# Performance work log

Measured on AMD Instinct MI355X. Metric: run time of the kernel, lower is better.

Reference implementation:

```python
import jax, jax.numpy as jnp
import numpy as np
import math

B, S, H = 2, 2048, 1024
NH, HD = 16, 64  # num heads, head dim; NH*HD == H


def setup_inputs() -> dict:
    key = jax.random.key(0)
    k1, k2, k3 = jax.random.split(key, 3)
    hidden_states = jax.random.normal(k1, (B, S, H), dtype=jnp.float32)
    # causal multiplicative mask [1,1,S,S], 1.0 where attending is allowed
    mask = jnp.tril(jnp.ones((S, S), dtype=jnp.float32))[None, None]
    W_qkv = jax.random.normal(k2, (H, 3 * H), dtype=jnp.float32) * (1.0 / math.sqrt(H))
    b_qkv = jnp.zeros((3 * H,), dtype=jnp.float32)
    W_out = jax.random.normal(k3, (H, H), dtype=jnp.float32) * (1.0 / math.sqrt(H))
    b_out = jnp.zeros((H,), dtype=jnp.float32)
    return {"hidden_states": hidden_states, "mask": mask, "W_qkv": W_qkv,
            "b_qkv": b_qkv, "W_out": W_out, "b_out": b_out}


def reference(hidden_states, mask, W_qkv, b_qkv, W_out, b_out):
    b, s, h = hidden_states.shape
    # fused QKV projection then split into contiguous thirds (split_tensor_along_last_dim)
    qkv = jnp.einsum('bsh,hd->bsd', hidden_states, W_qkv) + b_qkv
    q, k, v = jnp.split(qkv, 3, axis=-1)
    # [b, s, nh*hd] -> [b, nh, s, hd]
    def to_heads(t):
        return t.reshape(b, s, NH, HD).transpose(0, 2, 1, 3)
    q, k, v = to_heads(q), to_heads(k), to_heads(v)
    q = q / jnp.sqrt(jnp.float32(HD))  # scaling_attention_score=True
    scores = jnp.einsum('bhqd,bhkd->bhqk', q, k)  # [b,nh,s,s]
    # multiplicative mask + large-negative bias trick from standard_attention
    scores = scores * mask - 10000.0 * (1.0 - mask)
    probs = jax.nn.softmax(scores, axis=-1)
    ctx = jnp.einsum('bhqk,bhkd->bhqd', probs, v)
    ctx = ctx.transpose(0, 2, 1, 3).reshape(b, s, h)  # [b, s, nh*hd]
    return jnp.einsum('bsh,hd->bsd', ctx, W_out) + b_out
```

## Files before the change

kernel.cpp:

```cpp
#include <hip/hip_runtime.h>
#include <cstdint>
#include <cstddef>

#define NHEAD 16
#define HDIM 64
#define SEQ 2048
#define BATCH 2
#define HID 1024

typedef __bf16 bf16x8 __attribute__((ext_vector_type(8)));
typedef float f32x4 __attribute__((ext_vector_type(4)));

__device__ __forceinline__ unsigned short f2bf(float f) {
    union { float f; unsigned u; } v; v.f = f;
    unsigned r = v.u + 0x7fffu + ((v.u >> 16) & 1u);
    return (unsigned short)(r >> 16);
}

__global__ __launch_bounds__(256) void convert_f32_bf16(
    const float* __restrict__ in, unsigned short* __restrict__ out, int n) {
    int i = (blockIdx.x * 256 + threadIdx.x) * 8;
    if (i >= n) return;
    float4 a = *(const float4*)(in + i);
    float4 b = *(const float4*)(in + i + 4);
    uint4 o;
    o.x = (unsigned)f2bf(a.x) | ((unsigned)f2bf(a.y) << 16);
    o.y = (unsigned)f2bf(a.z) | ((unsigned)f2bf(a.w) << 16);
    o.z = (unsigned)f2bf(b.x) | ((unsigned)f2bf(b.y) << 16);
    o.w = (unsigned)f2bf(b.z) | ((unsigned)f2bf(b.w) << 16);
    *(uint4*)(out + i) = o;
}

__global__ __launch_bounds__(256) void transpose_f32_bf16(
    const float* __restrict__ in, unsigned short* __restrict__ out, int R, int C) {
    __shared__ unsigned short T[64][72];
    int t = threadIdx.x;
    int c0 = blockIdx.x * 64, r0 = blockIdx.y * 64;
    for (int p = 0; p < 4; ++p) {
        int idx = (p * 256 + t) * 4;
        int row = idx >> 6, col = idx & 63;
        float4 v = *(const float4*)(in + (size_t)(r0 + row) * C + c0 + col);
        T[row][col + 0] = f2bf(v.x);
        T[row][col + 1] = f2bf(v.y);
        T[row][col + 2] = f2bf(v.z);
        T[row][col + 3] = f2bf(v.w);
    }
    __syncthreads();
    for (int p = 0; p < 4; ++p) {
        int idx = (p * 256 + t) * 4;
        int orow = idx >> 6, ocol = idx & 63;
        ushort4 u;
        u.x = T[ocol + 0][orow];
        u.y = T[ocol + 1][orow];
        u.z = T[ocol + 2][orow];
        u.w = T[ocol + 3][orow];
        *(ushort4*)(out + (size_t)(c0 + orow) * R + r0 + ocol) = u;
    }
}

__global__ __launch_bounds__(256) void transpose_v(
    const unsigned short* __restrict__ in, unsigned short* __restrict__ out) {
    __shared__ unsigned short T[64][72];
    int t = threadIdx.x;
    int s0 = blockIdx.x * 64, bh = blockIdx.y;
    const unsigned short* ip = in + (size_t)bh * SEQ * HDIM;
    unsigned short* op = out + (size_t)bh * HDIM * SEQ;
    for (int p = 0; p < 2; ++p) {
        int idx = (p * 256 + t) * 8;
        int row = idx >> 6, col = idx & 63;
        *(uint4*)&T[row][col] = *(const uint4*)(ip + (size_t)(s0 + row) * HDIM + col);
    }
    __syncthreads();
    for (int p = 0; p < 4; ++p) {
        int idx = (p * 256 + t) * 4;
        int d = idx >> 6, c = idx & 63;
        ushort4 u;
        u.x = T[c + 0][d];
        u.y = T[c + 1][d];
        u.z = T[c + 2][d];
        u.w = T[c + 3][d];
        *(ushort4*)(op + (size_t)d * SEQ + s0 + c) = u;
    }
}

#define GEMM_BODY(Aptr, Btptr, KDIM)                                                     \
    __shared__ unsigned short As[128][32];                                               \
    __shared__ unsigned short Bs[128][32];                                               \
    int t = threadIdx.x;                                                                 \
    int wave = t >> 6, lane = t & 63, ln = lane & 15, quad = lane >> 4;                  \
    int wm = wave >> 1, wn = wave & 1;                                                   \
    int m0 = blockIdx.y * 128, n0 = blockIdx.x * 128;                                    \
    int srow = lane >> 2, scol = (lane & 3) * 8;                                         \
    f32x4 zero4 = {0.f, 0.f, 0.f, 0.f};                                                  \
    f32x4 acc[4][4];                                                                     \
    for (int mi = 0; mi < 4; ++mi)                                                       \
        for (int ni = 0; ni < 4; ++ni) acc[mi][ni] = zero4;                              \
    for (int kt = 0; kt < (KDIM); kt += 32) {                                            \
        for (int p = 0; p < 2; ++p) {                                                    \
            int r0 = (wave * 2 + p) * 16 + srow;                                         \
            __builtin_amdgcn_global_load_lds(                                            \
                (const __attribute__((address_space(1))) void*)                          \
                    ((Aptr) + (size_t)(m0 + r0) * (KDIM) + kt + scol),                   \
                (__attribute__((address_space(3))) void*)&As[(wave * 2 + p) * 16][0],    \
                16, 0, 0);                                                               \
            __builtin_amdgcn_global_load_lds(                                            \
                (const __attribute__((address_space(1))) void*)                          \
                    ((Btptr) + (size_t)(n0 + r0) * (KDIM) + kt + scol),                  \
                (__attribute__((address_space(3))) void*)&Bs[(wave * 2 + p) * 16][0],    \
                16, 0, 0);                                                               \
        }                                                                                \
        __syncthreads();                                                                 \
        bf16x8 af[4], bfr[4];                                                            \
        for (int mi = 0; mi < 4; ++mi)                                                   \
            af[mi] = *(const bf16x8*)&As[wm * 64 + mi * 16 + ln][quad * 8];              \
        for (int ni = 0; ni < 4; ++ni)                                                   \
            bfr[ni] = *(const bf16x8*)&Bs[wn * 64 + ni * 16 + ln][quad * 8];             \
        for (int mi = 0; mi < 4; ++mi)                                                   \
            for (int ni = 0; ni < 4; ++ni)                                               \
                acc[mi][ni] = __builtin_amdgcn_mfma_f32_16x16x32_bf16(                   \
                    af[mi], bfr[ni], acc[mi][ni], 0, 0, 0);                              \
        __syncthreads();                                                                 \
    }

__global__ __launch_bounds__(256) void gemm_qkv(
    const unsigned short* __restrict__ A, const unsigned short* __restrict__ Bt,
    const float* __restrict__ bias,
    unsigned short* __restrict__ Qb, unsigned short* __restrict__ Kb,
    unsigned short* __restrict__ Vtmp) {
    GEMM_BODY(A, Bt, 1024)
    int nbase = n0 + wn * 64;
    for (int ni = 0; ni < 4; ++ni) {
        int gn = nbase + ni * 16 + ln;
        float bv = bias[gn];
        int third = gn >> 10;
        int rem = gn & 1023;
        int h = rem >> 6, d = rem & 63;
        unsigned short* dst = third == 0 ? Qb : (third == 1 ? Kb : Vtmp);
        float scale = third == 0 ? 0.1803368801111f : 1.0f;
        for (int mi = 0; mi < 4; ++mi) {
            for (int r = 0; r < 4; ++r) {
                int gm = m0 + wm * 64 + mi * 16 + quad * 4 + r;
                int b = gm >> 11, s = gm & 2047;
                size_t bh = (size_t)(b * NHEAD + h);
                dst[(bh * SEQ + s) * HDIM + d] = f2bf((acc[mi][ni][r] + bv) * scale);
            }
        }
    }
}

__global__ __launch_bounds__(256) void gemm_out(
    const unsigned short* __restrict__ A, const unsigned short* __restrict__ Bt,
    const float* __restrict__ bias, float* __restrict__ C) {
    GEMM_BODY(A, Bt, 1024)
    int nbase = n0 + wn * 64;
    for (int ni = 0; ni < 4; ++ni) {
        int gn = nbase + ni * 16 + ln;
        float bv = bias[gn];
        for (int mi = 0; mi < 4; ++mi) {
            for (int r = 0; r < 4; ++r) {
                int gm = m0 + wm * 64 + mi * 16 + quad * 4 + r;
                C[(size_t)gm * HID + gn] = acc[mi][ni][r] + bv;
            }
        }
    }
}

__global__ __launch_bounds__(256) void flash_attn(
    const unsigned short* __restrict__ Qb, const unsigned short* __restrict__ Kb,
    const unsigned short* __restrict__ Vt, unsigned short* __restrict__ Ctx) {
    __shared__ unsigned short KsB[2][64][64];
    __shared__ unsigned short VsB[2][64][64];
    __shared__ unsigned short Ps[4][16][72];
    int tid = threadIdx.x;
    int wave = tid >> 6, lane = tid & 63, ln = lane & 15, quad = lane >> 4;
    int bx = blockIdx.x, bh = blockIdx.y;
    int qiA = bx;
    int q0A = qiA * 64, q0B = (31 - bx) * 64;
    const size_t baseQK = (size_t)bh * SEQ * HDIM;
    const size_t baseV = (size_t)bh * HDIM * SEQ;
    int b = bh >> 4, h = bh & 15;

    int rIn = lane >> 3;
    int gsw = ((lane & 7) ^ rIn) * 8;

    bf16x8 aqA0, aqA1, aqB0, aqB1;
    {
        const unsigned short* qp =
            Qb + baseQK + (size_t)(q0A + wave * 16 + ln) * HDIM + quad * 8;
        aqA0 = *(const bf16x8*)qp;
        aqA1 = *(const bf16x8*)(qp + 32);
        qp = Qb + baseQK + (size_t)(q0B + wave * 16 + ln) * HDIM + quad * 8;
        aqB0 = *(const bf16x8*)qp;
        aqB1 = *(const bf16x8*)(qp + 32);
    }
    bf16x8 aqc0 = aqA0, aqc1 = aqA1;

    auto prefetch = [&](int kj, int bi) {
        const unsigned short* kb = Kb + baseQK + (size_t)kj * 64 * HDIM;
        const unsigned short* vb = Vt + baseV + kj * 64;
        for (int c = wave; c < 8; c += 4) {
            __builtin_amdgcn_global_load_lds(
                (const __attribute__((address_space(1))) void*)(kb + (c * 8 + rIn) * HDIM + gsw),
                (__attribute__((address_space(3))) void*)&KsB[bi][c * 8][0], 16, 0, 0);
            __builtin_amdgcn_global_load_lds(
                (const __attribute__((address_space(1))) void*)(vb + (size_t)(c * 8 + rIn) * SEQ + gsw),
                (__attribute__((address_space(3))) void*)&VsB[bi][c * 8][0], 16, 0, 0);
        }
    };

    f32x4 zero4 = {0.f, 0.f, 0.f, 0.f};
    f32x4 o[4];
    float lacc = 0.f;
    for (int i = 0; i < 4; ++i) o[i] = zero4;

    prefetch(0, 0);
    for (int t = 0; t <= 32; ++t) {
        __syncthreads();
        if (t < 32) {
            int kn = (t + 1 <= qiA) ? (t + 1) : (t - qiA);
            prefetch(kn, (t + 1) & 1);
        }
        int buf = t & 1;
        bool diag = (t == qiA) || (t == 32);

        f32x4 s4[4];
        for (int ni = 0; ni < 4; ++ni) s4[ni] = zero4;
        for (int kk = 0; kk < 2; ++kk) {
            bf16x8 bq = kk ? aqc1 : aqc0;
            for (int ni = 0; ni < 4; ++ni) {
                bf16x8 ak = *(const bf16x8*)
                    &KsB[buf][ni * 16 + ln][(((kk * 4 + quad)) ^ (ln & 7)) * 8];
                s4[ni] = __builtin_amdgcn_mfma_f32_16x16x32_bf16(ak, bq, s4[ni], 0, 0, 0);
            }
        }
        if (diag) {
            for (int ni = 0; ni < 4; ++ni)
                for (int r = 0; r < 4; ++r)
                    if (ni * 16 + quad * 4 + r > wave * 16 + ln) s4[ni][r] = -1.0e38f;
        }

        for (int ni = 0; ni < 4; ++ni) {
            float e0 = __builtin_amdgcn_exp2f(s4[ni][0]);
            float e1 = __builtin_amdgcn_exp2f(s4[ni][1]);
            float e2 = __builtin_amdgcn_exp2f(s4[ni][2]);
            float e3 = __builtin_amdgcn_exp2f(s4[ni][3]);
            lacc += (e0 + e1) + (e2 + e3);
            ushort4 pk;
            pk.x = f2bf(e0); pk.y = f2bf(e1); pk.z = f2bf(e2); pk.w = f2bf(e3);
            *(ushort4*)&Ps[wave][ln][ni * 16 + quad * 4] = pk;
        }

        for (int kk = 0; kk < 2; ++kk) {
            bf16x8 bp = *(const bf16x8*)&Ps[wave][ln][kk * 32 + quad * 8];
            for (int ni = 0; ni < 4; ++ni) {
                bf16x8 av = *(const bf16x8*)
                    &VsB[buf][ni * 16 + ln][(((kk * 4 + quad)) ^ (ln & 7)) * 8];
                o[ni] = __builtin_amdgcn_mfma_f32_16x16x32_bf16(av, bp, o[ni], 0, 0, 0);
            }
        }

        if (diag) {
            float sum = lacc;
            sum += __shfl_xor(sum, 16);
            sum += __shfl_xor(sum, 32);
            float linv = __builtin_amdgcn_rcpf(sum);
            int q0 = (t == 32) ? q0B : q0A;
            size_t rowb = ((size_t)(b * SEQ + q0 + wave * 16 + ln)) * HID + h * 64;
            for (int ni = 0; ni < 4; ++ni) {
                ushort4 u;
                u.x = f2bf(o[ni][0] * linv);
                u.y = f2bf(o[ni][1] * linv);
                u.z = f2bf(o[ni][2] * linv);
                u.w = f2bf(o[ni][3] * linv);
                *(ushort4*)&Ctx[rowb + ni * 16 + quad * 4] = u;
            }
            for (int i = 0; i < 4; ++i) o[i] = zero4;
            lacc = 0.f;
            aqc0 = aqB0;
            aqc1 = aqB1;
        }
    }
}

extern "C" void kernel_launch(void* const* d_in, const int* in_sizes, int n_in,
                              void* d_out, int out_size, void* d_ws, size_t ws_size,
                              hipStream_t stream) {
    const float* X = (const float*)d_in[0];
    const float* Wqkv = (const float*)d_in[2];
    const float* bqkv = (const float*)d_in[3];
    const float* Wout = (const float*)d_in[4];
    const float* bout = (const float*)d_in[5];
    float* out = (float*)d_out;

    char* ws = (char*)d_ws;
    unsigned short* Xb   = (unsigned short*)(ws + 0);
    unsigned short* Vt   = (unsigned short*)(ws + 0);
    unsigned short* W1t  = (unsigned short*)(ws + 8388608);
    unsigned short* W2t  = (unsigned short*)(ws + 14680064);
    unsigned short* Qb   = (unsigned short*)(ws + 16777216);
    unsigned short* Kb   = (unsigned short*)(ws + 25165824);
    unsigned short* Vtmp = (unsigned short*)(ws + 33554432);
    unsigned short* Ctx  = (unsigned short*)(ws + 41943040);

    convert_f32_bf16<<<2048, 256, 0, stream>>>(X, Xb, 4194304);
    transpose_f32_bf16<<<dim3(48, 16), 256, 0, stream>>>(Wqkv, W1t, 1024, 3072);
    transpose_f32_bf16<<<dim3(16, 16), 256, 0, stream>>>(Wout, W2t, 1024, 1024);
    gemm_qkv<<<dim3(24, 32), 256, 0, stream>>>(Xb, W1t, bqkv, Qb, Kb, Vtmp);
    transpose_v<<<dim3(32, 32), 256, 0, stream>>>(Vtmp, Vt);
    flash_attn<<<dim3(16, 32), 256, 0, stream>>>(Qb, Kb, Vt, Ctx);
    gemm_out<<<dim3(8, 32), 256, 0, stream>>>(Ctx, W2t, bout, out);
}
```

Before: 209.4 us.

## Fuse V transpose into QKV GEMM, process paired query tiles jointly, remap blocks per XCD

The QKV GEMM epilogue now writes V directly in transposed layout, which removes the separate transpose_v kernel and its extra global round trip. The flash attention kernel now handles its two query tiles at the same time, so each K/V tile is loaded once and reused by both, where before the K range was walked twice in sequence. It also hoists the fragment loads, adds setprio around the MFMA blocks, uses the packed bf16 convert instruction, and sets launch bounds for two blocks per CU. All three main kernels remap block IDs so that neighbouring tiles land on the same XCD, aiming for better L2 reuse. Keeping both accumulators live raises register pressure, and the transposed V stores are narrow and strided.

```diff
diff --git a/kernel.cpp b/kernel.cpp
--- a/kernel.cpp
+++ b/kernel.cpp
@@ -15,6 +15,12 @@
     union { float f; unsigned u; } v; v.f = f;
     unsigned r = v.u + 0x7fffu + ((v.u >> 16) & 1u);
     return (unsigned short)(r >> 16);
+}
+
+__device__ __forceinline__ unsigned cvtpk_bf16(float a, float b) {
+    unsigned d;
+    asm("v_cvt_pk_bf16_f32 %0, %1, %2" : "=v"(d) : "v"(a), "v"(b));
+    return d;
 }
 
 __global__ __launch_bounds__(256) void convert_f32_bf16(
@@ -58,38 +64,13 @@
     }
 }
 
-__global__ __launch_bounds__(256) void transpose_v(
-    const unsigned short* __restrict__ in, unsigned short* __restrict__ out) {
-    __shared__ unsigned short T[64][72];
-    int t = threadIdx.x;
-    int s0 = blockIdx.x * 64, bh = blockIdx.y;
-    const unsigned short* ip = in + (size_t)bh * SEQ * HDIM;
-    unsigned short* op = out + (size_t)bh * HDIM * SEQ;
-    for (int p = 0; p < 2; ++p) {
-        int idx = (p * 256 + t) * 8;
-        int row = idx >> 6, col = idx & 63;
-        *(uint4*)&T[row][col] = *(const uint4*)(ip + (size_t)(s0 + row) * HDIM + col);
-    }
-    __syncthreads();
-    for (int p = 0; p < 4; ++p) {
-        int idx = (p * 256 + t) * 4;
-        int d = idx >> 6, c = idx & 63;
-        ushort4 u;
-        u.x = T[c + 0][d];
-        u.y = T[c + 1][d];
-        u.z = T[c + 2][d];
-        u.w = T[c + 3][d];
-        *(ushort4*)(op + (size_t)d * SEQ + s0 + c) = u;
-    }
-}
-
-#define GEMM_BODY(Aptr, Btptr, KDIM)                                                     \
+#define GEMM_BODY(Aptr, Btptr, KDIM, BX, BY)                                             \
     __shared__ unsigned short As[128][32];                                               \
     __shared__ unsigned short Bs[128][32];                                               \
     int t = threadIdx.x;                                                                 \
     int wave = t >> 6, lane = t & 63, ln = lane & 15, quad = lane >> 4;                  \
     int wm = wave >> 1, wn = wave & 1;                                                   \
-    int m0 = blockIdx.y * 128, n0 = blockIdx.x * 128;                                    \
+    int m0 = (BY) * 128, n0 = (BX) * 128;                                                \
     int srow = lane >> 2, scol = (lane & 3) * 8;                                         \
     f32x4 zero4 = {0.f, 0.f, 0.f, 0.f};                                                  \
     f32x4 acc[4][4];                                                                     \
@@ -126,8 +107,12 @@
     const unsigned short* __restrict__ A, const unsigned short* __restrict__ Bt,
     const float* __restrict__ bias,
     unsigned short* __restrict__ Qb, unsigned short* __restrict__ Kb,
-    unsigned short* __restrict__ Vtmp) {
-    GEMM_BODY(A, Bt, 1024)
+    unsigned short* __restrict__ Vt) {
+    int fid = blockIdx.y * 24 + blockIdx.x;
+    int xcd = fid & 7, jj = fid >> 3;
+    int by = (xcd & 3) * 8 + jj / 12;
+    int bx = (xcd >> 2) * 12 + jj % 12;
+    GEMM_BODY(A, Bt, 1024, bx, by)
     int nbase = n0 + wn * 64;
     for (int ni = 0; ni < 4; ++ni) {
         int gn = nbase + ni * 16 + ln;
@@ -135,14 +120,28 @@
         int third = gn >> 10;
         int rem = gn & 1023;
         int h = rem >> 6, d = rem & 63;
-        unsigned short* dst = third == 0 ? Qb : (third == 1 ? Kb : Vtmp);
-        float scale = third == 0 ? 0.1803368801111f : 1.0f;
-        for (int mi = 0; mi < 4; ++mi) {
-            for (int r = 0; r < 4; ++r) {
-                int gm = m0 + wm * 64 + mi * 16 + quad * 4 + r;
+        if (third == 2) {
+            for (int mi = 0; mi < 4; ++mi) {
+                int gm = m0 + wm * 64 + mi * 16 + quad * 4;
                 int b = gm >> 11, s = gm & 2047;
                 size_t bh = (size_t)(b * NHEAD + h);
-                dst[(bh * SEQ + s) * HDIM + d] = f2bf((acc[mi][ni][r] + bv) * scale);
+                ushort4 u;
+                u.x = f2bf(acc[mi][ni][0] + bv);
+                u.y = f2bf(acc[mi][ni][1] + bv);
+                u.z = f2bf(acc[mi][ni][2] + bv);
+                u.w = f2bf(acc[mi][ni][3] + bv);
+                *(ushort4*)&Vt[(bh * HDIM + d) * SEQ + s] = u;
+            }
+        } else {
+            unsigned short* dst = third == 0 ? Qb : Kb;
+            float scale = third == 0 ? 0.1803368801111f : 1.0f;
+            for (int mi = 0; mi < 4; ++mi) {
+                for (int r = 0; r < 4; ++r) {
+                    int gm = m0 + wm * 64 + mi * 16 + quad * 4 + r;
+                    int b = gm >> 11, s = gm & 2047;
+                    size_t bh = (size_t)(b * NHEAD + h);
+                    dst[(bh * SEQ + s) * HDIM + d] = f2bf((acc[mi][ni][r] + bv) * scale);
+                }
             }
         }
     }
@@ -151,7 +150,11 @@
 __global__ __launch_bounds__(256) void gemm_out(
     const unsigned short* __restrict__ A, const unsigned short* __restrict__ Bt,
     const float* __restrict__ bias, float* __restrict__ C) {
-    GEMM_BODY(A, Bt, 1024)
+    int fid = blockIdx.y * 8 + blockIdx.x;
+    int xcd = fid & 7, jj = fid >> 3;
+    int by = xcd * 4 + (jj >> 3);
+    int bx = jj & 7;
+    GEMM_BODY(A, Bt, 1024, bx, by)
     int nbase = n0 + wn * 64;
     for (int ni = 0; ni < 4; ++ni) {
         int gn = nbase + ni * 16 + ln;
@@ -165,17 +168,23 @@
     }
 }
 
-__global__ __launch_bounds__(256) void flash_attn(
+__global__ __launch_bounds__(256, 2) void flash_attn(
     const unsigned short* __restrict__ Qb, const unsigned short* __restrict__ Kb,
     const unsigned short* __restrict__ Vt, unsigned short* __restrict__ Ctx) {
     __shared__ unsigned short KsB[2][64][64];
     __shared__ unsigned short VsB[2][64][64];
-    __shared__ unsigned short Ps[4][16][72];
+    __shared__ unsigned short Ps[2][4][16][72];
     int tid = threadIdx.x;
     int wave = tid >> 6, lane = tid & 63, ln = lane & 15, quad = lane >> 4;
-    int bx = blockIdx.x, bh = blockIdx.y;
-    int qiA = bx;
-    int q0A = qiA * 64, q0B = (31 - bx) * 64;
+
+    int id = blockIdx.y * 16 + blockIdx.x;
+    int xcd = id & 7, j = id >> 3;
+    int bh = xcd * 4 + (j & 3);
+    int r0 = (j >> 2) & 7;
+    int bxrole = (j < 32) ? r0 : 15 - r0;
+    int qiA = bxrole;
+    int qiB = 31 - bxrole;
+    int q0A = qiA * 64, q0B = qiB * 64;
     const size_t baseQK = (size_t)bh * SEQ * HDIM;
     const size_t baseV = (size_t)bh * HDIM * SEQ;
     int b = bh >> 4, h = bh & 15;
@@ -193,7 +202,6 @@
         aqB0 = *(const bf16x8*)qp;
         aqB1 = *(const bf16x8*)(qp + 32);
     }
-    bf16x8 aqc0 = aqA0, aqc1 = aqA1;
 
     auto prefetch = [&](int kj, int bi) {
         const unsigned short* kb = Kb + baseQK + (size_t)kj * 64 * HDIM;
@@ -209,76 +217,138 @@
     };
 
     f32x4 zero4 = {0.f, 0.f, 0.f, 0.f};
-    f32x4 o[4];
-    float lacc = 0.f;
-    for (int i = 0; i < 4; ++i) o[i] = zero4;
+    f32x4 oA[4], oB[4];
+    float laccA = 0.f, laccB = 0.f;
+    for (int i = 0; i < 4; ++i) { oA[i] = zero4; oB[i] = zero4; }
+
+    auto epilogue = [&](const f32x4* o, float lacc, int q0) {
+        float sum = lacc;
+        sum += __shfl_xor(sum, 16);
+        sum += __shfl_xor(sum, 32);
+        float linv = __builtin_amdgcn_rcpf(sum);
+        size_t rowb = ((size_t)(b * SEQ + q0 + wave * 16 + ln)) * HID + h * 64;
+        for (int ni = 0; ni < 4; ++ni) {
+            ushort4 u;
+            u.x = f2bf(o[ni][0] * linv);
+            u.y = f2bf(o[ni][1] * linv);
+            u.z = f2bf(o[ni][2] * linv);
+            u.w = f2bf(o[ni][3] * linv);
+            *(ushort4*)&Ctx[rowb + ni * 16 + quad * 4] = u;
+        }
+    };
 
     prefetch(0, 0);
-    for (int t = 0; t <= 32; ++t) {
+    for (int t = 0; t <= qiB; ++t) {
         __syncthreads();
-        if (t < 32) {
-            int kn = (t + 1 <= qiA) ? (t + 1) : (t - qiA);
-            prefetch(kn, (t + 1) & 1);
-        }
+        if (t < qiB) prefetch(t + 1, (t + 1) & 1);
         int buf = t & 1;
-        bool diag = (t == qiA) || (t == 32);
-
-        f32x4 s4[4];
-        for (int ni = 0; ni < 4; ++ni) s4[ni] = zero4;
+        bool joint = (t <= qiA);
+
+        bf16x8 akf[2][4];
+#pragma unroll
+        for (int kk = 0; kk < 2; ++kk)
+#pragma unroll
+            for (int ni = 0; ni < 4; ++ni)
+                akf[kk][ni] = *(const bf16x8*)
+                    &KsB[buf][ni * 16 + ln][((kk * 4 + quad) ^ (ln & 7)) * 8];
+        f32x4 sA[4], sB[4];
+#pragma unroll
+        for (int ni = 0; ni < 4; ++ni) { sA[ni] = zero4; sB[ni] = zero4; }
+        __builtin_amdgcn_s_setprio(1);
+#pragma unroll
         for (int kk = 0; kk < 2; ++kk) {
-            bf16x8 bq = kk ? aqc1 : aqc0;
+            bf16x8 bq = kk ? aqB1 : aqB0;
+#pragma unroll
+            for (int ni = 0; ni < 4; ++ni)
+                sB[ni] = __builtin_amdgcn_mfma_f32_16x16x32_bf16(akf[kk][ni], bq, sB[ni], 0, 0, 0);
+        }
+        if (joint) {
+#pragma unroll
+            for (int kk = 0; kk < 2; ++kk) {
+                bf16x8 bq = kk ? aqA1 : aqA0;
+#pragma unroll
+                for (int ni = 0; ni < 4; ++ni)
+                    sA[ni] = __builtin_amdgcn_mfma_f32_16x16x32_bf16(akf[kk][ni], bq, sA[ni], 0, 0, 0);
+            }
+        }
+        __builtin_amdgcn_s_setprio(0);
+
+        if (t == qiB) {
+#pragma unroll
+            for (int ni = 0; ni < 4; ++ni)
+#pragma unroll
+                for (int r = 0; r < 4; ++r)
+                    if (ni * 16 + quad * 4 + r > wave * 16 + ln) sB[ni][r] = -1.0e38f;
+        }
+        if (t == qiA) {
+#pragma unroll
+            for (int ni = 0; ni < 4; ++ni)
+#pragma unroll
+                for (int r = 0; r < 4; ++r)
+                    if (ni * 16 + quad * 4 + r > wave * 16 + ln) sA[ni][r] = -1.0e38f;
+        }
+
+#pragma unroll
+        for (int ni = 0; ni < 4; ++ni) {
+            float e0 = __builtin_amdgcn_exp2f(sB[ni][0]);
+            float e1 = __builtin_amdgcn_exp2f(sB[ni][1]);
+            float e2 = __builtin_amdgcn_exp2f(sB[ni][2]);
+            float e3 = __builtin_amdgcn_exp2f(sB[ni][3]);
+            laccB += (e0 + e1) + (e2 + e3);
+            uint2 pw;
+            pw.x = cvtpk_bf16(e0, e1);
+            pw.y = cvtpk_bf16(e2, e3);
+            *(uint2*)&Ps[0][wave][ln][ni * 16 + quad * 4] = pw;
+        }
+        if (joint) {
+#pragma unroll
             for (int ni = 0; ni < 4; ++ni) {
-                bf16x8 ak = *(const bf16x8*)
-                    &KsB[buf][ni * 16 + ln][(((kk * 4 + quad)) ^ (ln & 7)) * 8];
-                s4[ni] = __builtin_amdgcn_mfma_f32_16x16x32_bf16(ak, bq, s4[ni], 0, 0, 0);
-            }
-        }
-        if (diag) {
-            for (int ni = 0; ni < 4; ++ni)
-                for (int r = 0; r < 4; ++r)
-                    if (ni * 16 + quad * 4 + r > wave * 16 + ln) s4[ni][r] = -1.0e38f;
-        }
-
-        for (int ni = 0; ni < 4; ++ni) {
-            float e0 = __builtin_amdgcn_exp2f(s4[ni][0]);
-            float e1 = __builtin_amdgcn_exp2f(s4[ni][1]);
-            float e2 = __builtin_amdgcn_exp2f(s4[ni][2]);
-            float e3 = __builtin_amdgcn_exp2f(s4[ni][3]);
-            lacc += (e0 + e1) + (e2 + e3);
-            ushort4 pk;
-            pk.x = f2bf(e0); pk.y = f2bf(e1); pk.z = f2bf(e2); pk.w = f2bf(e3);
-            *(ushort4*)&Ps[wave][ln][ni * 16 + quad * 4] = pk;
-        }
-
-        for (int kk = 0; kk < 2; ++kk) {
-            bf16x8 bp = *(const bf16x8*)&Ps[wave][ln][kk * 32 + quad * 8];
-            for (int ni = 0; ni < 4; ++ni) {
-                bf16x8 av = *(const bf16x8*)
-                    &VsB[buf][ni * 16 + ln][(((kk * 4 + quad)) ^ (ln & 7)) * 8];
-                o[ni] = __builtin_amdgcn_mfma_f32_16x16x32_bf16(av, bp, o[ni], 0, 0, 0);
-            }
-        }
-
-        if (diag) {
-            float sum = lacc;
-            sum += __shfl_xor(sum, 16);
-            sum += __shfl_xor(sum, 32);
-            float linv = __builtin_amdgcn_rcpf(sum);
-            int q0 = (t == 32) ? q0B : q0A;
-            size_t rowb = ((size_t)(b * SEQ + q0 + wave * 16 + ln)) * HID + h * 64;
-            for (int ni = 0; ni < 4; ++ni) {
-                ushort4 u;
-                u.x = f2bf(o[ni][0] * linv);
-                u.y = f2bf(o[ni][1] * linv);
-                u.z = f2bf(o[ni][2] * linv);
-                u.w = f2bf(o[ni][3] * linv);
-                *(ushort4*)&Ctx[rowb + ni * 16 + quad * 4] = u;
-            }
-            for (int i = 0; i < 4; ++i) o[i] = zero4;
-            lacc = 0.f;
-            aqc0 = aqB0;
-            aqc1 = aqB1;
-        }
+                float e0 = __builtin_amdgcn_exp2f(sA[ni][0]);
+                float e1 = __builtin_amdgcn_exp2f(sA[ni][1]);
+                float e2 = __builtin_amdgcn_exp2f(sA[ni][2]);
+                float e3 = __builtin_amdgcn_exp2f(sA[ni][3]);
+                laccA += (e0 + e1) + (e2 + e3);
+                uint2 pw;
+                pw.x = cvtpk_bf16(e0, e1);
+                pw.y = cvtpk_bf16(e2, e3);
+                *(uint2*)&Ps[1][wave][ln][ni * 16 + quad * 4] = pw;
+            }
+        }
+
+        bf16x8 avf[2][4];
+#pragma unroll
+        for (int kk = 0; kk < 2; ++kk)
+#pragma unroll
+            for (int ni = 0; ni < 4; ++ni)
+                avf[kk][ni] = *(const bf16x8*)
+                    &VsB[buf][ni * 16 + ln][((kk * 4 + quad) ^ (ln & 7)) * 8];
+        {
+            bf16x8 bp0 = *(const bf16x8*)&Ps[0][wave][ln][quad * 8];
+            bf16x8 bp1 = *(const bf16x8*)&Ps[0][wave][ln][32 + quad * 8];
+            __builtin_amdgcn_s_setprio(1);
+#pragma unroll
+            for (int ni = 0; ni < 4; ++ni)
+                oB[ni] = __builtin_amdgcn_mfma_f32_16x16x32_bf16(avf[0][ni], bp0, oB[ni], 0, 0, 0);
+#pragma unroll
+            for (int ni = 0; ni < 4; ++ni)
+                oB[ni] = __builtin_amdgcn_mfma_f32_16x16x32_bf16(avf[1][ni], bp1, oB[ni], 0, 0, 0);
+            __builtin_amdgcn_s_setprio(0);
+        }
+        if (joint) {
+            bf16x8 bp0 = *(const bf16x8*)&Ps[1][wave][ln][quad * 8];
+            bf16x8 bp1 = *(const bf16x8*)&Ps[1][wave][ln][32 + quad * 8];
+            __builtin_amdgcn_s_setprio(1);
+#pragma unroll
+            for (int ni = 0; ni < 4; ++ni)
+                oA[ni] = __builtin_amdgcn_mfma_f32_16x16x32_bf16(avf[0][ni], bp0, oA[ni], 0, 0, 0);
+#pragma unroll
+            for (int ni = 0; ni < 4; ++ni)
+                oA[ni] = __builtin_amdgcn_mfma_f32_16x16x32_bf16(avf[1][ni], bp1, oA[ni], 0, 0, 0);
+            __builtin_amdgcn_s_setprio(0);
+        }
+
+        if (t == qiA) epilogue(oA, laccA, q0A);
+        if (t == qiB) epilogue(oB, laccB, q0B);
     }
 }
 
@@ -294,19 +364,17 @@
 
     char* ws = (char*)d_ws;
     unsigned short* Xb   = (unsigned short*)(ws + 0);
-    unsigned short* Vt   = (unsigned short*)(ws + 0);
     unsigned short* W1t  = (unsigned short*)(ws + 8388608);
     unsigned short* W2t  = (unsigned short*)(ws + 14680064);
     unsigned short* Qb   = (unsigned short*)(ws + 16777216);
     unsigned short* Kb   = (unsigned short*)(ws + 25165824);
-    unsigned short* Vtmp = (unsigned short*)(ws + 33554432);
+    unsigned short* Vt   = (unsigned short*)(ws + 33554432);
     unsigned short* Ctx  = (unsigned short*)(ws + 41943040);
 
     convert_f32_bf16<<<2048, 256, 0, stream>>>(X, Xb, 4194304);
     transpose_f32_bf16<<<dim3(48, 16), 256, 0, stream>>>(Wqkv, W1t, 1024, 3072);
     transpose_f32_bf16<<<dim3(16, 16), 256, 0, stream>>>(Wout, W2t, 1024, 1024);
-    gemm_qkv<<<dim3(24, 32), 256, 0, stream>>>(Xb, W1t, bqkv, Qb, Kb, Vtmp);
-    transpose_v<<<dim3(32, 32), 256, 0, stream>>>(Vtmp, Vt);
+    gemm_qkv<<<dim3(24, 32), 256, 0, stream>>>(Xb, W1t, bqkv, Qb, Kb, Vt);
     flash_attn<<<dim3(16, 32), 256, 0, stream>>>(Qb, Kb, Vt, Ctx);
     gemm_out<<<dim3(8, 32), 256, 0, stream>>>(Ctx, W2t, bout, out);
 }
```

Result: no change. 206.0 us (-1.6%).
